# Performance work log

Measured on AMD Instinct MI355X. Metric: run time of the kernel, lower is better.

## Reference

```python
import jax, jax.numpy as jnp
import numpy as np

HEAD_NUM = 16
EMBED = 1024

def setup_inputs() -> dict:
    key = jax.random.key(0)
    k1, k2, k3 = jax.random.split(key, 3)
    x = jax.random.normal(k1, (2, 2048, EMBED), dtype=jnp.float32)
    W_qkv = jax.random.normal(k2, (3 * EMBED, EMBED), dtype=jnp.float32) * (EMBED ** -0.5)
    W_out = jax.random.normal(k3, (EMBED, EMBED), dtype=jnp.float32) * (EMBED ** -0.5)
    return {"x": x, "W_qkv": W_qkv, "W_out": W_out}

def reference(x, W_qkv, W_out):
    b, t, E = x.shape
    h = HEAD_NUM
    d = E // h
    dk = (E / h) ** 0.5
    qkv = x @ W_qkv.T  # [b, t, 3E]
    # einops 'b t (d k h) -> k b h t d' with k=3, h=head_num (d outermost in the split)
    qkv = qkv.reshape(b, t, d, 3, h).transpose(3, 0, 4, 1, 2)  # [3, b, h, t, d]
    q, k, v = qkv[0], qkv[1], qkv[2]
    energy = jnp.einsum('bhid,bhjd->bhij', q, k) / dk  # [b, h, t, t]
    attn = jax.nn.softmax(energy, axis=-1)
    out = jnp.einsum('bhij,bhjd->bhid', attn, v)  # [b, h, t, d]
    out = out.transpose(0, 2, 1, 3).reshape(b, t, E)  # 'b h t d -> b t (h d)'
    return out @ W_out.T
```

## Files before the change

### kernel.cpp

```cpp
#include <hip/hip_runtime.h>
#include <hip/hip_bf16.h>


#define HEADS 16
#define EMB   1024
#define HDIM  64
#define BB    2
#define TT    2048
#define QSCALE 0.18033688011112042f

typedef __attribute__((ext_vector_type(8)))  short      bf16x8;
typedef __attribute__((ext_vector_type(8)))  _Float16   f16x8;
typedef __attribute__((ext_vector_type(4)))  float      f32x4;
typedef __attribute__((ext_vector_type(16))) float      f32x16;
typedef __attribute__((ext_vector_type(4)))  unsigned   u32x4;

__device__ __forceinline__ unsigned short f2bf(float f) {
    __hip_bfloat16 h = __float2bfloat16(f);
    return __builtin_bit_cast(unsigned short, h);
}
__device__ __forceinline__ float fexp2(float x) {
#if __has_builtin(__builtin_amdgcn_exp2f)
    return __builtin_amdgcn_exp2f(x);
#else
    return exp2f(x);
#endif
}
__device__ __forceinline__ unsigned pkrtz(float a, float b) {
    auto r = __builtin_amdgcn_cvt_pkrtz(a, b);
    return __builtin_bit_cast(unsigned, r);
}
__device__ __forceinline__ unsigned short f2h(float f) {
    return (unsigned short)(pkrtz(f, 0.f) & 0xffffu);
}
__device__ __forceinline__ float h2f(unsigned short u) {
    return (float)__builtin_bit_cast(_Float16, u);
}
__device__ __forceinline__ void gload_lds16(const void* g, void* l) {
    __builtin_amdgcn_global_load_lds(
        (const __attribute__((address_space(1))) void*)g,
        (__attribute__((address_space(3))) void*)l, 16, 0, 0);
}
__device__ __forceinline__ int swzi(int row, int blk) {
    return row * 64 + ((blk ^ (row & 7)) << 3);
}
__device__ __forceinline__ void pl32swap(unsigned& a, unsigned& b) {
    asm("v_permlane32_swap_b32 %0, %1" : "+v"(a), "+v"(b));
}

__global__ __launch_bounds__(256)
void conv_all(const float* __restrict__ x,    unsigned short* __restrict__ xb,
              const float* __restrict__ Wqkv, unsigned short* __restrict__ Wqb,
              const float* __restrict__ Wout, unsigned short* __restrict__ Wob) {
    const int blk = blockIdx.x;
    if (blk < 2048) {
        const int i = blk * 256 + threadIdx.x;
        const float4 v0 = ((const float4*)x)[i * 2];
        const float4 v1 = ((const float4*)x)[i * 2 + 1];
        ushort4 a, b;
        a.x = f2bf(v0.x); a.y = f2bf(v0.y); a.z = f2bf(v0.z); a.w = f2bf(v0.w);
        b.x = f2bf(v1.x); b.y = f2bf(v1.y); b.z = f2bf(v1.z); b.w = f2bf(v1.w);
        ((ushort4*)xb)[i * 2]     = a;
        ((ushort4*)xb)[i * 2 + 1] = b;
    } else if (blk < 5120) {
        const int np = blk - 2048;
        const int ns = (np & 63) * 48 + (np >> 10) * 16 + ((np >> 6) & 15);
        const float4 v = ((const float4*)(Wqkv + (size_t)ns * 1024))[threadIdx.x];
        ushort4 u;
        u.x = f2bf(v.x); u.y = f2bf(v.y); u.z = f2bf(v.z); u.w = f2bf(v.w);
        ((ushort4*)(Wqb + (size_t)np * 1024))[threadIdx.x] = u;
    } else {
        const int np = blk - 5120;
        const float4 v = ((const float4*)(Wout + (size_t)np * 1024))[threadIdx.x];
        ushort4 u;
        u.x = f2bf(v.x); u.y = f2bf(v.y); u.z = f2bf(v.z); u.w = f2bf(v.w);
        ((ushort4*)(Wob + (size_t)np * 1024))[threadIdx.x] = u;
    }
}

__global__ __launch_bounds__(512, 2)
void gemm256_qkv(const unsigned short* __restrict__ Ag,
                 const unsigned short* __restrict__ Wg,
                 unsigned short* __restrict__ QKb,
                 unsigned short* __restrict__ Vt) {
    __shared__ __align__(16) unsigned short AbL[2][256 * 64];
    __shared__ __align__(16) unsigned short BbL[2][192 * 64];

    const int tid = threadIdx.x, lane = tid & 63, w = tid >> 6;
    const int n0 = blockIdx.x * 192, m0 = blockIdx.y * 256;
    const int wm = (w >> 2) * 128;
    const int wn = (w & 3) * 48;
    const int r16 = lane & 15, g = lane >> 4, gq = g * 4;

    f32x4 acc[8][3];
    #pragma unroll
    for (int i = 0; i < 8; ++i)
        #pragma unroll
        for (int j = 0; j < 3; ++j)
            acc[i][j] = (f32x4){0.f, 0.f, 0.f, 0.f};

    const int srl = lane >> 3;
    const int scol = ((lane & 7) ^ srl) << 3;
    const unsigned short* Asrc = Ag + (size_t)(m0 + w * 32 + srl) * 1024 + scol;
    const unsigned short* Bsrc = Wg + (size_t)(n0 + w * 24 + srl) * 1024 + scol;

#define STAGE256(AB, BB, K0)                                                \
    do {                                                                    \
        _Pragma("unroll")                                                   \
        for (int i = 0; i < 4; ++i)                                         \
            gload_lds16(Asrc + (K0) + i * 8192,                             \
                        (AB) + (w * 32 + i * 8) * 64);                      \
        _Pragma("unroll")                                                   \
        for (int i = 0; i < 3; ++i)                                         \
            gload_lds16(Bsrc + (K0) + i * 8192,                             \
                        (BB) + (w * 24 + i * 8) * 64);                      \
    } while (0)

    unsigned short *pa0 = &AbL[0][0], *pa1 = &AbL[1][0];
    unsigned short *pb0 = &BbL[0][0], *pb1 = &BbL[1][0];

    STAGE256(pa0, pb0, 0);

    for (int kt = 0; kt < 16; ++kt) {
        asm volatile("s_waitcnt vmcnt(0)" ::: "memory");
        __builtin_amdgcn_s_barrier();
        if (kt < 15) STAGE256(pa1, pb1, (kt + 1) * 64);

        __builtin_amdgcn_s_setprio(1);
        #pragma unroll
        for (int ks = 0; ks < 2; ++ks) {
            bf16x8 bf[3];
            #pragma unroll
            for (int ni = 0; ni < 3; ++ni)
                bf[ni] = *(const bf16x8*)&pb0[swzi(wn + ni * 16 + r16, ks * 4 + g)];
            #pragma unroll
            for (int mi = 0; mi < 8; ++mi) {
                const bf16x8 xf = *(const bf16x8*)&pa0[swzi(wm + mi * 16 + r16, ks * 4 + g)];
                #pragma unroll
                for (int ni = 0; ni < 3; ++ni)
                    acc[mi][ni] = __builtin_amdgcn_mfma_f32_16x16x32_bf16(
                        bf[ni], xf, acc[mi][ni], 0, 0, 0);
            }
        }
        __builtin_amdgcn_s_setprio(0);

        unsigned short* t;
        t = pa0; pa0 = pa1; pa1 = t;
        t = pb0; pb0 = pb1; pb1 = t;
    }
#undef STAGE256

    #pragma unroll
    for (int ni = 0; ni < 3; ++ni) {
        const int npb = n0 + wn + ni * 16;
        if (npb < 2048) {
            const float qs = npb < 1024 ? QSCALE : 1.0f;
            #pragma unroll
            for (int mi = 0; mi < 8; ++mi) {
                const int m = m0 + wm + mi * 16 + r16;
                ushort4 u;
                u.x = f2bf(acc[mi][ni][0] * qs); u.y = f2bf(acc[mi][ni][1] * qs);
                u.z = f2bf(acc[mi][ni][2] * qs); u.w = f2bf(acc[mi][ni][3] * qs);
                *(ushort4*)&QKb[(size_t)m * 2048 + npb + gq] = u;
            }
        } else {
            #pragma unroll
            for (int mi = 0; mi < 8; ++mi) {
                const int m  = m0 + wm + mi * 16 + r16;
                const int b  = m >> 11, tt = m & 2047;
                const int nv0 = npb - 2048 + gq;
                #pragma unroll
                for (int j = 0; j < 4; ++j) {
                    const int nv = nv0 + j, h = nv >> 6, d = nv & 63;
                    Vt[(((size_t)(b * HEADS + h)) * HDIM + d) * TT + tt] =
                        f2h(acc[mi][ni][j]);
                }
            }
        }
    }
}

__global__ __launch_bounds__(256)
void gemm_bf16(const unsigned short* __restrict__ Ag,
               const unsigned short* __restrict__ Wg,
               float* __restrict__ Cout) {
    __shared__ __align__(16) unsigned short AbL[2][128 * 32];
    __shared__ __align__(16) unsigned short WbL[2][128 * 32];

    const int tid = threadIdx.x, lane = tid & 63, w = tid >> 6;
    const int n0 = blockIdx.x * 128, m0 = blockIdx.y * 128;
    const int wn = (w >> 1) * 64, wm = (w & 1) * 64;
    const int r16 = lane & 15, g = lane >> 4;
    const int goff = ((g ^ ((r16 >> 1) & 3)) << 3);

    f32x4 acc[4][4];
    #pragma unroll
    for (int i = 0; i < 4; ++i)
        #pragma unroll
        for (int j = 0; j < 4; ++j)
            acc[i][j] = (f32x4){0.f, 0.f, 0.f, 0.f};

    const int srow = w * 16 + (lane >> 2);
    const int scol = ((lane & 3) ^ ((lane >> 3) & 3)) << 3;
    const int sdst = (w * 16) * 32;
    const unsigned short* Asrc = Ag + (size_t)(m0 + srow) * 1024 + scol;
    const unsigned short* Wsrc = Wg + (size_t)(n0 + srow) * 1024 + scol;

#define STAGE(AB, WB, K0)                                            \
    do {                                                             \
        gload_lds16(Asrc + (K0),              (AB) + sdst);          \
        gload_lds16(Asrc + (K0) + 64 * 1024,  (AB) + sdst + 2048);   \
        gload_lds16(Wsrc + (K0),              (WB) + sdst);          \
        gload_lds16(Wsrc + (K0) + 64 * 1024,  (WB) + sdst + 2048);   \
    } while (0)

    unsigned short *pa0 = &AbL[0][0], *pa1 = &AbL[1][0];
    unsigned short *pw0 = &WbL[0][0], *pw1 = &WbL[1][0];

    STAGE(pa0, pw0, 0);

    for (int kt = 0; kt < 32; ++kt) {
        asm volatile("s_waitcnt vmcnt(0)" ::: "memory");
        __builtin_amdgcn_s_barrier();
        if (kt < 31) STAGE(pa1, pw1, (kt + 1) * 32);

        bf16x8 xf[4];
        #pragma unroll
        for (int mi = 0; mi < 4; ++mi)
            xf[mi] = *(const bf16x8*)&pa0[(wm + mi * 16 + r16) * 32 + goff];
        __builtin_amdgcn_s_setprio(1);
        #pragma unroll
        for (int ni = 0; ni < 4; ++ni) {
            const bf16x8 wf = *(const bf16x8*)&pw0[(wn + ni * 16 + r16) * 32 + goff];
            #pragma unroll
            for (int mi = 0; mi < 4; ++mi)
                acc[ni][mi] = __builtin_amdgcn_mfma_f32_16x16x32_bf16(
                    wf, xf[mi], acc[ni][mi], 0, 0, 0);
        }
        __builtin_amdgcn_s_setprio(0);

        unsigned short* t;
        t = pa0; pa0 = pa1; pa1 = t;
        t = pw0; pw0 = pw1; pw1 = t;
    }
#undef STAGE

    const int gq = g * 4;
    #pragma unroll
    for (int ni = 0; ni < 4; ++ni)
        #pragma unroll
        for (int mi = 0; mi < 4; ++mi) {
            const int m = m0 + wm + mi * 16 + r16;
            *(f32x4*)&Cout[(size_t)m * 1024 + (n0 + wn + ni * 16 + gq)] =
                acc[ni][mi];
        }
}

__global__ __launch_bounds__(256, 4)
void attn32(const unsigned short* __restrict__ QKb,
            const unsigned short* __restrict__ Vt,
            unsigned short* __restrict__ PO0,
            unsigned short* __restrict__ PO1,
            float* __restrict__ PL0,
            float* __restrict__ PL1) {
    __shared__ __align__(16) unsigned short Ks[2][64 * 64];
    __shared__ __align__(16) unsigned short Vs[2][64 * 64];

    const int tid = threadIdx.x, lane = tid & 63, w = tid >> 6;
    const int l31 = lane & 31, hi = lane >> 5;
    const int bid = blockIdx.x + 32 * blockIdx.y + 512 * blockIdx.z;
    const int vb  = (bid & 7) * 128 + (bid >> 3);
    const int qt  = vb & 15, kh = (vb >> 4) & 1;
    const int h   = (vb >> 5) & 15, b = vb >> 9;
    const int kbase = kh * 1024;
    const unsigned short* Vsrc = Vt + (size_t)(b * HEADS + h) * HDIM * TT;
    unsigned short* PO = kh ? PO1 : PO0;
    float*          PL = kh ? PL1 : PL0;

    bf16x8 qf[4];
    {
        const unsigned short* qrow =
            QKb + ((size_t)(b * TT + qt * 128 + w * 32 + l31)) * 2048 + h * HDIM;
        #pragma unroll
        for (int dc = 0; dc < 4; ++dc)
            qf[dc] = *(const bf16x8*)(qrow + dc * 16 + hi * 8);
    }

    const f32x16 zz = {};
    f32x16 o0 = {}, o1 = {};
    float lrun = 0.f;

    const int srl = lane >> 3;
    const int scb = lane & 7;
    const int cbs = (scb ^ srl) << 3;
    const int rl0 = w * 16 + srl;
    const unsigned short* kp0 =
        QKb + (size_t)(b * TT + kbase + rl0) * 2048 + 1024 + h * HDIM + cbs;
    const unsigned short* kp1 = kp0 + (size_t)8 * 2048;
    const unsigned short* vp0 = Vsrc + (size_t)rl0 * TT + kbase + cbs;
    const unsigned short* vp1 = vp0 + (size_t)8 * TT;
    unsigned short* const kd0 = &Ks[0][(w * 16) * 64];
    unsigned short* const kd1 = &Ks[1][(w * 16) * 64];
    unsigned short* const vd0 = &Vs[0][(w * 16) * 64];
    unsigned short* const vd1 = &Vs[1][(w * 16) * 64];

#define STAGE(KD, VD)                                                  \
    do {                                                               \
        gload_lds16(kp0, (KD));        gload_lds16(kp1, (KD) + 512);   \
        gload_lds16(vp0, (VD));        gload_lds16(vp1, (VD) + 512);   \
        kp0 += 64 * 2048; kp1 += 64 * 2048; vp0 += 64; vp1 += 64;      \
    } while (0)

    STAGE(kd0, vd0);

    for (int jt = 0; jt < 16; ++jt) {
        const int bb = jt & 1;
        __syncthreads();
        if (jt < 15) {
            if (bb) STAGE(kd0, vd0); else STAGE(kd1, vd1);
        }
        const unsigned short* KsB = &Ks[bb][0];
        const unsigned short* VsB = &Vs[bb][0];

        f32x16 stA, stB;
        __builtin_amdgcn_s_setprio(1);
        #pragma unroll
        for (int dc = 0; dc < 4; ++dc) {
            const bf16x8 kaA = *(const bf16x8*)&KsB[swzi(l31,      dc * 2 + hi)];
            const bf16x8 kaB = *(const bf16x8*)&KsB[swzi(32 + l31, dc * 2 + hi)];
            if (dc == 0) {
                stA = __builtin_amdgcn_mfma_f32_32x32x16_bf16(kaA, qf[0], zz, 0, 0, 0);
                stB = __builtin_amdgcn_mfma_f32_32x32x16_bf16(kaB, qf[0], zz, 0, 0, 0);
            } else {
                stA = __builtin_amdgcn_mfma_f32_32x32x16_bf16(kaA, qf[dc], stA, 0, 0, 0);
                stB = __builtin_amdgcn_mfma_f32_32x32x16_bf16(kaB, qf[dc], stB, 0, 0, 0);
            }
        }
        __builtin_amdgcn_s_setprio(0);

        #pragma unroll
        for (int x = 0; x < 2; ++x) {
            const f32x16& st = x ? stB : stA;
            float sum;
            unsigned wd[8];
            #pragma unroll
            for (int c = 0; c < 4; ++c) {
                const float e0 = fexp2(st[4 * c + 0]);
                const float e1 = fexp2(st[4 * c + 1]);
                const float e2 = fexp2(st[4 * c + 2]);
                const float e3 = fexp2(st[4 * c + 3]);
                const float s4 = (e0 + e1) + (e2 + e3);
                sum = c ? sum + s4 : s4;
                wd[2 * c]     = pkrtz(e0, e1);
                wd[2 * c + 1] = pkrtz(e2, e3);
            }
            lrun += sum;

            unsigned a0 = wd[0], a2 = wd[2];  pl32swap(a0, a2);
            unsigned a1 = wd[1], a3 = wd[3];  pl32swap(a1, a3);
            unsigned b0 = wd[4], b2 = wd[6];  pl32swap(b0, b2);
            unsigned b1 = wd[5], b3 = wd[7];  pl32swap(b1, b3);
            const u32x4 fva = {a0, a1, a2, a3};
            const u32x4 fvb = {b0, b1, b2, b3};
            const f16x8 pa0 = __builtin_bit_cast(f16x8, fva);
            const f16x8 pa1 = __builtin_bit_cast(f16x8, fvb);

            const int f0 = 2 * x;
            __builtin_amdgcn_s_setprio(1);
            {
                const f16x8 vb00 = *(const f16x8*)&VsB[swzi(l31,      f0 * 2 + hi)];
                const f16x8 vb01 = *(const f16x8*)&VsB[swzi(32 + l31, f0 * 2 + hi)];
                o0 = __builtin_amdgcn_mfma_f32_32x32x16_f16(pa0, vb00, o0, 0, 0, 0);
                o1 = __builtin_amdgcn_mfma_f32_32x32x16_f16(pa0, vb01, o1, 0, 0, 0);
                const f16x8 vb10 = *(const f16x8*)&VsB[swzi(l31,      (f0 + 1) * 2 + hi)];
                const f16x8 vb11 = *(const f16x8*)&VsB[swzi(32 + l31, (f0 + 1) * 2 + hi)];
                o0 = __builtin_amdgcn_mfma_f32_32x32x16_f16(pa1, vb10, o0, 0, 0, 0);
                o1 = __builtin_amdgcn_mfma_f32_32x32x16_f16(pa1, vb11, o1, 0, 0, 0);
            }
            __builtin_amdgcn_s_setprio(0);
        }
    }
#undef STAGE

    lrun += __shfl_xor(lrun, 32);
    const float inv = 1.0f / lrun;
    #pragma unroll
    for (int r = 0; r < 16; ++r) {
        const int qr = (r & 3) + 8 * (r >> 2) + 4 * hi;
        const float ir = __shfl(inv, qr);
        const int q = qt * 128 + w * 32 + qr;
        unsigned short* dst = PO + ((size_t)(b * TT + q)) * EMB + h * HDIM + l31;
        dst[0]  = f2h(o0[r] * ir);
        dst[32] = f2h(o1[r] * ir);
    }
    if (!hi) {
        const int q = qt * 128 + w * 32 + l31;
        PL[((size_t)(b * HEADS + h)) * TT + q] = lrun;
    }
}

__global__ __launch_bounds__(256)
void merge_attn(const unsigned short* __restrict__ PO0,
                const unsigned short* __restrict__ PO1,
                const float* __restrict__ PL0,
                const float* __restrict__ PL1,
                unsigned short* __restrict__ AOb) {
    const int i = blockIdx.x * 256 + threadIdx.x;
    const int tg  = i >> 8;
    const int col = (i & 255) * 4;
    const int h   = col >> 6;
    const int b   = tg >> 11, t = tg & 2047;

    const float la = PL0[((size_t)(b * HEADS + h)) * TT + t];
    const float lb = PL1[((size_t)(b * HEADS + h)) * TT + t];
    const float inv = 1.0f / (la + lb);
    const float wa = la * inv, wb = lb * inv;

    const ushort4 a = ((const ushort4*)PO0)[i];
    const ushort4 c = ((const ushort4*)PO1)[i];
    ushort4 o;
    o.x = f2bf(h2f(a.x) * wa + h2f(c.x) * wb);
    o.y = f2bf(h2f(a.y) * wa + h2f(c.y) * wb);
    o.z = f2bf(h2f(a.z) * wa + h2f(c.z) * wb);
    o.w = f2bf(h2f(a.w) * wa + h2f(c.w) * wb);
    ((ushort4*)AOb)[i] = o;
}

extern "C" void kernel_launch(void* const* d_in, const int* in_sizes, int n_in,
                              void* d_out, int out_size, void* d_ws, size_t ws_size,
                              hipStream_t stream) {
    const float* x    = (const float*)d_in[0];
    const float* Wqkv = (const float*)d_in[1];
    const float* Wout = (const float*)d_in[2];
    float* out = (float*)d_out;

    unsigned short* Wqb = (unsigned short*)d_ws;
    unsigned short* Wob = Wqb + 3145728;
    unsigned short* xb  = Wob + 1048576;
    unsigned short* QKb = xb  + 4194304;
    unsigned short* Vt  = QKb + 8388608;
    unsigned short* PO0 = Vt  + 4194304;
    unsigned short* PO1 = PO0 + 4194304;
    float*          PL0 = (float*)(PO1 + 4194304);
    float*          PL1 = PL0 + 65536;
    unsigned short* AOb = xb;

    conv_all<<<6144, 256, 0, stream>>>(x, xb, Wqkv, Wqb, Wout, Wob);

    gemm256_qkv<<<dim3(16, 16), 512, 0, stream>>>(xb, Wqb, QKb, Vt);

    attn32<<<dim3(32, 16, 2), 256, 0, stream>>>(QKb, Vt, PO0, PO1, PL0, PL1);

    merge_attn<<<4096, 256, 0, stream>>>(PO0, PO1, PL0, PL1, AOb);

    gemm_bf16<<<dim3(8, 32), 256, 0, stream>>>(AOb, Wob, out);
}
```

Before: 126.1 us.

## Triple-buffer QKV GEMM with K=32 stages and XCD-aware block remapping

The QKV projection GEMM moves from a double buffer with a K-step of 64 to a triple-buffered pipeline with a K-step of 32. Loads run two stages ahead, and a partial vmcnt wait lets the next tile's load overlap the current MFMA work. Both GEMMs now use a 1D grid remapped so consecutive blocks on the same XCD share A/B tiles, aiming for better L2 reuse. The cost is more barriers per K loop and a new swizzle layout, with only some waves issuing the B loads.

```diff
diff --git a/kernel.cpp b/kernel.cpp
--- a/kernel.cpp
+++ b/kernel.cpp
@@ -43,6 +43,9 @@
 }
 __device__ __forceinline__ int swzi(int row, int blk) {
     return row * 64 + ((blk ^ (row & 7)) << 3);
+}
+__device__ __forceinline__ int swz32(int row, int blk) {
+    return row * 32 + ((blk ^ ((row >> 1) & 3)) << 3);
 }
 __device__ __forceinline__ void pl32swap(unsigned& a, unsigned& b) {
     asm("v_permlane32_swap_b32 %0, %1" : "+v"(a), "+v"(b));
@@ -83,11 +86,14 @@
                  const unsigned short* __restrict__ Wg,
                  unsigned short* __restrict__ QKb,
                  unsigned short* __restrict__ Vt) {
-    __shared__ __align__(16) unsigned short AbL[2][256 * 64];
-    __shared__ __align__(16) unsigned short BbL[2][192 * 64];
+    __shared__ __align__(16) unsigned short AbL[3][256 * 32];
+    __shared__ __align__(16) unsigned short BbL[3][192 * 32];
 
     const int tid = threadIdx.x, lane = tid & 63, w = tid >> 6;
-    const int n0 = blockIdx.x * 192, m0 = blockIdx.y * 256;
+    const int bid = blockIdx.x;
+    const int vb  = (bid & 7) * 32 + (bid >> 3);
+    const int n0  = (vb >> 4) * 192;
+    const int m0  = (vb & 15) * 256;
     const int wm = (w >> 2) * 128;
     const int wn = (w & 3) * 48;
     const int r16 = lane & 15, g = lane >> 4, gq = g * 4;
@@ -99,54 +105,57 @@
         for (int j = 0; j < 3; ++j)
             acc[i][j] = (f32x4){0.f, 0.f, 0.f, 0.f};
 
-    const int srl = lane >> 3;
-    const int scol = ((lane & 7) ^ srl) << 3;
-    const unsigned short* Asrc = Ag + (size_t)(m0 + w * 32 + srl) * 1024 + scol;
-    const unsigned short* Bsrc = Wg + (size_t)(n0 + w * 24 + srl) * 1024 + scol;
-
-#define STAGE256(AB, BB, K0)                                                \
+    const int drow = lane >> 2;
+    const int sblk = (lane & 3) ^ ((drow >> 1) & 3);
+    const int scol = sblk << 3;
+    const unsigned short* Asrc = Ag + (size_t)(m0 + w * 32 + drow) * 1024 + scol;
+    const unsigned short* Bsrc = Wg + (size_t)(n0 + w * 32 + drow) * 1024 + scol;
+
+#define STAGE256(BUF, K0)                                                   \
     do {                                                                    \
-        _Pragma("unroll")                                                   \
-        for (int i = 0; i < 4; ++i)                                         \
-            gload_lds16(Asrc + (K0) + i * 8192,                             \
-                        (AB) + (w * 32 + i * 8) * 64);                      \
-        _Pragma("unroll")                                                   \
-        for (int i = 0; i < 3; ++i)                                         \
-            gload_lds16(Bsrc + (K0) + i * 8192,                             \
-                        (BB) + (w * 24 + i * 8) * 64);                      \
+        gload_lds16(Asrc + (K0),             &AbL[BUF][(w * 32) * 32]);     \
+        gload_lds16(Asrc + (K0) + 16 * 1024, &AbL[BUF][(w * 32 + 16) * 32]);\
+        if (w < 6) {                                                        \
+            gload_lds16(Bsrc + (K0),             &BbL[BUF][(w * 32) * 32]); \
+            gload_lds16(Bsrc + (K0) + 16 * 1024, &BbL[BUF][(w * 32 + 16) * 32]); \
+        }                                                                   \
     } while (0)
 
-    unsigned short *pa0 = &AbL[0][0], *pa1 = &AbL[1][0];
-    unsigned short *pb0 = &BbL[0][0], *pb1 = &BbL[1][0];
-
-    STAGE256(pa0, pb0, 0);
-
-    for (int kt = 0; kt < 16; ++kt) {
-        asm volatile("s_waitcnt vmcnt(0)" ::: "memory");
+    STAGE256(0, 0);
+    STAGE256(1, 32);
+
+    int cur = 0;
+    for (int kt = 0; kt < 32; ++kt) {
+        if (kt < 31) {
+            if (w < 6) asm volatile("s_waitcnt vmcnt(4)" ::: "memory");
+            else       asm volatile("s_waitcnt vmcnt(2)" ::: "memory");
+        } else {
+            asm volatile("s_waitcnt vmcnt(0)" ::: "memory");
+        }
         __builtin_amdgcn_s_barrier();
-        if (kt < 15) STAGE256(pa1, pb1, (kt + 1) * 64);
-
+        if (kt < 30) {
+            const int nb = (cur + 2) % 3;
+            STAGE256(nb, (kt + 2) * 32);
+        }
+
+        const unsigned short* Ab = &AbL[cur][0];
+        const unsigned short* Bb = &BbL[cur][0];
+        bf16x8 bfr[3];
+        #pragma unroll
+        for (int ni = 0; ni < 3; ++ni)
+            bfr[ni] = *(const bf16x8*)&Bb[swz32(wn + ni * 16 + r16, g)];
         __builtin_amdgcn_s_setprio(1);
         #pragma unroll
-        for (int ks = 0; ks < 2; ++ks) {
-            bf16x8 bf[3];
+        for (int mi = 0; mi < 8; ++mi) {
+            const bf16x8 xf = *(const bf16x8*)&Ab[swz32(wm + mi * 16 + r16, g)];
             #pragma unroll
             for (int ni = 0; ni < 3; ++ni)
-                bf[ni] = *(const bf16x8*)&pb0[swzi(wn + ni * 16 + r16, ks * 4 + g)];
-            #pragma unroll
-            for (int mi = 0; mi < 8; ++mi) {
-                const bf16x8 xf = *(const bf16x8*)&pa0[swzi(wm + mi * 16 + r16, ks * 4 + g)];
-                #pragma unroll
-                for (int ni = 0; ni < 3; ++ni)
-                    acc[mi][ni] = __builtin_amdgcn_mfma_f32_16x16x32_bf16(
-                        bf[ni], xf, acc[mi][ni], 0, 0, 0);
-            }
+                acc[mi][ni] = __builtin_amdgcn_mfma_f32_16x16x32_bf16(
+                    bfr[ni], xf, acc[mi][ni], 0, 0, 0);
         }
         __builtin_amdgcn_s_setprio(0);
 
-        unsigned short* t;
-        t = pa0; pa0 = pa1; pa1 = t;
-        t = pb0; pb0 = pb1; pb1 = t;
+        cur = (cur + 1) % 3;
     }
 #undef STAGE256
 
@@ -188,7 +197,10 @@
     __shared__ __align__(16) unsigned short WbL[2][128 * 32];
 
     const int tid = threadIdx.x, lane = tid & 63, w = tid >> 6;
-    const int n0 = blockIdx.x * 128, m0 = blockIdx.y * 128;
+    const int bid = blockIdx.x;
+    const int vb  = (bid & 7) * 32 + (bid >> 3);
+    const int n0  = (vb >> 5) * 128;
+    const int m0  = (vb & 31) * 128;
     const int wn = (w >> 1) * 64, wm = (w & 1) * 64;
     const int r16 = lane & 15, g = lane >> 4;
     const int goff = ((g ^ ((r16 >> 1) & 3)) << 3);
@@ -447,11 +459,11 @@
 
     conv_all<<<6144, 256, 0, stream>>>(x, xb, Wqkv, Wqb, Wout, Wob);
 
-    gemm256_qkv<<<dim3(16, 16), 512, 0, stream>>>(xb, Wqb, QKb, Vt);
+    gemm256_qkv<<<256, 512, 0, stream>>>(xb, Wqb, QKb, Vt);
 
     attn32<<<dim3(32, 16, 2), 256, 0, stream>>>(QKb, Vt, PO0, PO1, PL0, PL1);
 
     merge_attn<<<4096, 256, 0, stream>>>(PO0, PO1, PL0, PL1, AOb);
 
-    gemm_bf16<<<dim3(8, 32), 256, 0, stream>>>(AOb, Wob, out);
-}
+    gemm_bf16<<<256, 256, 0, stream>>>(AOb, Wob, out);
+}
```

Result: slower. 133.9 us (+6.2%).
